# Kernel optimization log

Measured on AMD Instinct MI355X. Metric: run time of the kernel, lower is better.

## Reference

```python
import jax, jax.numpy as jnp
import numpy as np

B, C, H, W = 2, 256, 64, 64
NUM_HEADS = 8


def setup_inputs() -> dict:
    key = jax.random.key(0)
    k1, k2, k3 = jax.random.split(key, 3)
    x = jax.random.normal(k1, (B, C, H, W), dtype=jnp.float32)
    # 1x1 convs, bias=False -> plain [out_ch, in_ch] matrices
    w_qkv = jax.random.normal(k2, (3 * C, C), dtype=jnp.float32) * (1.0 / np.sqrt(C))
    w_proj = jax.random.normal(k3, (C, C), dtype=jnp.float32) * (1.0 / np.sqrt(C))
    return {"x": x, "w_qkv": w_qkv, "w_proj": w_proj}


def reference(x, w_qkv, w_proj):
    b, c, h, w = x.shape
    hd = NUM_HEADS
    d = c // hd  # head dim
    n = h * w    # number of tokens

    # 1x1 conv == channel matmul: [3C, C] x [B, C, H, W] -> [B, 3C, H, W]
    qkv = jnp.einsum('oc,bchw->bohw', w_qkv, x)
    q, k, v = jnp.split(qkv, 3, axis=1)

    def reshape(t):
        return t.reshape(b, hd, d, n)  # [B, h, d, N]

    q, k, v = map(reshape, (q, k, v))

    # scores[b,h,i,j] = sum_d q[b,h,d,i] * k[b,h,d,j] / sqrt(d)
    scores = jnp.einsum('bhdi,bhdj->bhij', q, k) / jnp.sqrt(jnp.asarray(d, x.dtype))
    attn = jax.nn.softmax(scores, axis=-1)

    # out[b,h,d,i] = sum_j attn[b,h,i,j] * v[b,h,d,j]
    out = jnp.einsum('bhij,bhdj->bhdi', attn, v)
    out = out.reshape(b, c, h, w)

    return jnp.einsum('oc,bchw->bohw', w_proj, out) + x
```

## Files before the change

### kernel.cpp

```cpp
#include <hip/hip_runtime.h>
#include <hip/hip_bf16.h>

#define NB  2
#define CC  256
#define NHD 8
#define HD  32
#define NT  4096

typedef __bf16 bf16x8 __attribute__((ext_vector_type(8)));
typedef bf16x8 bf16x8_ma __attribute__((may_alias));
typedef __bf16 bf16x4 __attribute__((ext_vector_type(4)));
typedef bf16x4 bf16x4_ma __attribute__((may_alias));
typedef float  f32x4  __attribute__((ext_vector_type(4)));
typedef float  f32x16 __attribute__((ext_vector_type(16)));
typedef unsigned int u32x4 __attribute__((ext_vector_type(4)));

static __device__ __forceinline__ f32x4 zero4() {
    f32x4 z = {0.f, 0.f, 0.f, 0.f}; return z;
}
static __device__ __forceinline__ f32x16 zero16() {
    f32x16 z = {0.f,0.f,0.f,0.f,0.f,0.f,0.f,0.f,
                0.f,0.f,0.f,0.f,0.f,0.f,0.f,0.f};
    return z;
}

#define QSCALE 0.25505392421795654f

#define CVT_PK(dst, lo, hi_) \
    asm("v_cvt_pk_bf16_f32 %0, %1, %2" : "=v"(dst) : "v"(lo), "v"(hi_))
#define PLSWAP(x, y) \
    asm("v_permlane32_swap_b32 %0, %1" : "+v"(x), "+v"(y))


__global__ __launch_bounds__(256) void convw_k(const float* __restrict__ s1,
                                               __bf16* __restrict__ d1, int n1,
                                               const float* __restrict__ s2,
                                               __bf16* __restrict__ d2, int n2) {
    const int i = blockIdx.x * 256 + threadIdx.x;
    if (i < n1) d1[i] = (__bf16)s1[i];
    else if (i - n1 < n2) d2[i - n1] = (__bf16)s2[i - n1];
}

__global__ __launch_bounds__(256) void transpose_k(const float* __restrict__ x,
                                                   __bf16* __restrict__ xt) {
    __shared__ __bf16 T[64][65];
    const int tid = threadIdx.x;
    const int n0 = blockIdx.x * 64, c0 = blockIdx.y * 64, b = blockIdx.z;

#pragma unroll
    for (int rep = 0; rep < 16; ++rep) {
        const int e = rep * 256 + tid;
        const int cl = e >> 6, nl = e & 63;
        T[nl][cl] = (__bf16)x[((size_t)(b * CC + c0 + cl)) * NT + n0 + nl];
    }
    __syncthreads();
#pragma unroll
    for (int rep = 0; rep < 16; ++rep) {
        const int e = rep * 256 + tid;
        const int nl = e >> 6, cl = e & 63;
        xt[((size_t)(b * NT + n0 + nl)) * CC + c0 + cl] = T[nl][cl];
    }
}

__global__ __launch_bounds__(256) void qkv_k(const __bf16* __restrict__ wqkv,
                                             const __bf16* __restrict__ xt,
                                             __bf16* __restrict__ qt,
                                             __bf16* __restrict__ kt,
                                             __bf16* __restrict__ vv) {
    const int lane = threadIdx.x & 63, wv = threadIdx.x >> 6;
    const int g = lane >> 4, c16 = lane & 15;
    const int b    = blockIdx.z;
    const int o0   = blockIdx.y * 64 + wv * 16;
    const int tok0 = blockIdx.x * 64;

    const __bf16* arow = wqkv + (size_t)(o0 + c16) * CC + g * 8;
    const __bf16* brow = xt + ((size_t)(b * NT + tok0 + c16)) * CC + g * 8;

    f32x4 acc[4];
#pragma unroll
    for (int i = 0; i < 4; ++i) acc[i] = zero4();

#pragma unroll
    for (int k0 = 0; k0 < CC; k0 += 32) {
        bf16x8 a = *(const bf16x8_ma*)(arow + k0);
#pragma unroll
        for (int js = 0; js < 4; ++js) {
            bf16x8 bb = *(const bf16x8_ma*)(brow + (size_t)js * 16 * CC + k0);
            acc[js] = __builtin_amdgcn_mfma_f32_16x16x32_bf16(a, bb, acc[js], 0, 0, 0);
        }
    }

    const int reg = o0 >> 8;
    const int oo0 = (o0 & 255) + g * 4;
    const int h   = oo0 >> 5;
    const int dd0 = oo0 & 31;
    const size_t bh = (size_t)(b * NHD + h);

#pragma unroll
    for (int js = 0; js < 4; ++js) {
        const int tok = tok0 + js * 16 + c16;
        if (reg == 0) {
            bf16x4 pk;
#pragma unroll
            for (int r = 0; r < 4; ++r) pk[r] = (__bf16)(acc[js][r] * QSCALE);
            *(bf16x4_ma*)(qt + (bh * NT + tok) * HD + dd0) = pk;
        } else if (reg == 1) {
            bf16x4 pk;
#pragma unroll
            for (int r = 0; r < 4; ++r) pk[r] = (__bf16)acc[js][r];
            *(bf16x4_ma*)(kt + (bh * NT + tok) * HD + dd0) = pk;
        } else {
#pragma unroll
            for (int r = 0; r < 4; ++r)
                vv[(bh * HD + dd0 + r) * NT + tok] = (__bf16)acc[js][r];
        }
    }
}

__global__ __launch_bounds__(256, 2) void attn_k(const __bf16* __restrict__ qt,
                                                 const __bf16* __restrict__ kt,
                                                 const __bf16* __restrict__ vv,
                                                 __bf16* __restrict__ ao) {
    __shared__ __align__(16) __bf16 KF[2][2][2][512];
    __shared__ __align__(16) __bf16 VF[2][2][2][512];

    const int tid  = threadIdx.x;
    const int lane = tid & 63, wv = tid >> 6;
    const int c32 = lane & 31, hi = lane >> 5;
    const int bh = blockIdx.y;
    const int b = bh >> 3, h = bh & 7;
    const int i0q = blockIdx.x * 128 + wv * 32;

    const __bf16* qbase = qt + ((size_t)bh * NT + i0q) * HD;
    const __bf16* kbase = kt + (size_t)bh * NT * HD;
    const __bf16* vbase = vv + (size_t)bh * HD * NT;

    const int stg_js = wv & 1, stg_sl = wv >> 1;

    bf16x8 aq0 = *(const bf16x8_ma*)(qbase + (size_t)c32 * HD + hi * 8);
    bf16x8 aq1 = *(const bf16x8_ma*)(qbase + (size_t)c32 * HD + 16 + hi * 8);

    f32x16 oacc = zero16();
    float rsa[4] = {0.f, 0.f, 0.f, 0.f};

#define STAGE(bf, jb) do {                                                              \
    const __bf16* gk = kbase + (size_t)((jb) + stg_js * 32 + c32) * HD                  \
                             + stg_sl * 16 + hi * 8;                                    \
    __builtin_amdgcn_global_load_lds(                                                   \
        (const __attribute__((address_space(1))) void*)gk,                              \
        (__attribute__((address_space(3))) void*)&KF[bf][stg_js][stg_sl][0],            \
        16, 0, 0);                                                                      \
    const __bf16* gv = vbase + (size_t)c32 * NT + (jb) + stg_js * 32                    \
                             + stg_sl * 16 + hi * 8;                                    \
    __builtin_amdgcn_global_load_lds(                                                   \
        (const __attribute__((address_space(1))) void*)gv,                              \
        (__attribute__((address_space(3))) void*)&VF[bf][stg_js][stg_sl][0],            \
        16, 0, 0);                                                                      \
} while (0)

#define SUBTILE(bf, js) do {                                                            \
    bf16x8 fk0 = *(const bf16x8_ma*)&KF[bf][js][0][lane * 8];                           \
    bf16x8 fk1 = *(const bf16x8_ma*)&KF[bf][js][1][lane * 8];                           \
    bf16x8 fv0 = *(const bf16x8_ma*)&VF[bf][js][0][lane * 8];                           \
    bf16x8 fv1 = *(const bf16x8_ma*)&VF[bf][js][1][lane * 8];                           \
    f32x16 s = __builtin_amdgcn_mfma_f32_32x32x16_bf16(fk0, aq0, zero16(), 0, 0, 0);    \
    s = __builtin_amdgcn_mfma_f32_32x32x16_bf16(fk1, aq1, s, 0, 0, 0);                  \
    float p[16];                                                                        \
    _Pragma("unroll")                                                                   \
    for (int r = 0; r < 16; ++r) {                                                      \
        p[r] = __builtin_amdgcn_exp2f(s[r]);                                            \
        rsa[r & 3] += p[r];                                                             \
    }                                                                                   \
    unsigned pk[8];                                                                     \
    _Pragma("unroll")                                                                   \
    for (int i = 0; i < 8; ++i) CVT_PK(pk[i], p[2 * i], p[2 * i + 1]);                  \
    PLSWAP(pk[0], pk[2]);                                                               \
    PLSWAP(pk[1], pk[3]);                                                               \
    PLSWAP(pk[4], pk[6]);                                                               \
    PLSWAP(pk[5], pk[7]);                                                               \
    u32x4 a0 = {pk[0], pk[1], pk[2], pk[3]};                                            \
    u32x4 a1 = {pk[4], pk[5], pk[6], pk[7]};                                            \
    const bf16x8 ap0 = __builtin_bit_cast(bf16x8, a0);                                  \
    const bf16x8 ap1 = __builtin_bit_cast(bf16x8, a1);                                  \
    oacc = __builtin_amdgcn_mfma_f32_32x32x16_bf16(ap0, fv0, oacc, 0, 0, 0);            \
    oacc = __builtin_amdgcn_mfma_f32_32x32x16_bf16(ap1, fv1, oacc, 0, 0, 0);            \
} while (0)

    const int NTILES = NT / 64;

    STAGE(0, 0);
    asm volatile("s_waitcnt vmcnt(0)" ::: "memory");
    __syncthreads();

    int buf = 0;
#pragma unroll 1
    for (int t = 0; t < NTILES; ++t) {
        if (t + 1 < NTILES) STAGE(buf ^ 1, (t + 1) * 64);
        SUBTILE(buf, 0);
        SUBTILE(buf, 1);
        asm volatile("s_waitcnt vmcnt(0)" ::: "memory");
        __syncthreads();
        buf ^= 1;
    }

#undef STAGE
#undef SUBTILE

    float rs = (rsa[0] + rsa[1]) + (rsa[2] + rsa[3]);
    rs += __shfl_xor(rs, 32, 64);

#pragma unroll
    for (int g4 = 0; g4 < 4; ++g4) {
#pragma unroll
        for (int r = 0; r < 4; ++r) {
            const int q = 8 * g4 + 4 * hi + r;
            const float lt = __shfl(rs, q, 64);
            ao[((size_t)(b * NT) + i0q + q) * CC + h * HD + c32] =
                (__bf16)(oacc[4 * g4 + r] / lt);
        }
    }
}

__global__ __launch_bounds__(256) void proj_k(const __bf16* __restrict__ wp,
                                              const __bf16* __restrict__ ao,
                                              const float* __restrict__ x,
                                              float* __restrict__ out) {
    const int lane = threadIdx.x & 63, wv = threadIdx.x >> 6;
    const int g = lane >> 4, c16 = lane & 15;
    const int b    = blockIdx.z;
    const int o0   = blockIdx.y * 64 + wv * 16;
    const int tok0 = blockIdx.x * 64;

    const __bf16* arow = wp + (size_t)(o0 + c16) * CC + g * 8;
    const __bf16* brow = ao + ((size_t)(b * NT + tok0 + c16)) * CC + g * 8;

    f32x4 acc[4];
#pragma unroll
    for (int i = 0; i < 4; ++i) acc[i] = zero4();

#pragma unroll
    for (int k0 = 0; k0 < CC; k0 += 32) {
        bf16x8 a = *(const bf16x8_ma*)(arow + k0);
#pragma unroll
        for (int js = 0; js < 4; ++js) {
            bf16x8 bb = *(const bf16x8_ma*)(brow + (size_t)js * 16 * CC + k0);
            acc[js] = __builtin_amdgcn_mfma_f32_16x16x32_bf16(a, bb, acc[js], 0, 0, 0);
        }
    }

#pragma unroll
    for (int js = 0; js < 4; ++js) {
        const int tok = tok0 + js * 16 + c16;
#pragma unroll
        for (int r = 0; r < 4; ++r) {
            const int o = o0 + g * 4 + r;
            const size_t idx = ((size_t)(b * CC + o)) * NT + tok;
            out[idx] = acc[js][r] + x[idx];
        }
    }
}

extern "C" void kernel_launch(void* const* d_in, const int* in_sizes, int n_in,
                              void* d_out, int out_size, void* d_ws, size_t ws_size,
                              hipStream_t stream) {
    const int SX  = NB * CC * NT;
    const int SW3 = 3 * CC * CC;
    const int SW1 = CC * CC;
    const size_t E = (size_t)SX;

    const float* x  = nullptr;
    const float* wq = nullptr;
    const float* wp = nullptr;
    for (int i = 0; i < n_in; ++i) {
        const int sz = in_sizes[i];
        if (sz == SX || sz == 2 * SX || sz == 4 * SX)           x  = (const float*)d_in[i];
        else if (sz == SW3 || sz == 2 * SW3 || sz == 4 * SW3)   wq = (const float*)d_in[i];
        else if (sz == SW1 || sz == 2 * SW1 || sz == 4 * SW1)   wp = (const float*)d_in[i];
    }
    if (!x || !wq || !wp) {
        x  = (const float*)d_in[0];
        wq = (const float*)d_in[1];
        wp = (const float*)d_in[2];
    }

    __bf16* ws  = (__bf16*)d_ws;
    __bf16* wqb = ws;
    __bf16* wpb = wqb + SW3;
    __bf16* xt  = wpb + SW1;
    __bf16* qt  = xt + E;
    __bf16* kt  = qt + E;
    __bf16* vv  = kt + E;
    __bf16* ao  = xt;

    float* out = (float*)d_out;

    convw_k<<<dim3((SW3 + SW1 + 255) / 256), 256, 0, stream>>>(wq, wqb, SW3, wp, wpb, SW1);
    transpose_k<<<dim3(NT / 64, CC / 64, NB), 256, 0, stream>>>(x, xt);
    qkv_k<<<dim3(NT / 64, (3 * CC) / 64, NB), 256, 0, stream>>>(wqb, xt, qt, kt, vv);
    attn_k<<<dim3(NT / 128, NB * NHD), 256, 0, stream>>>(qt, kt, vv, ao);
    proj_k<<<dim3(NT / 64, CC / 64, NB), 256, 0, stream>>>(wpb, ao, x, out);
}
```

Before: 166.5 us.

## Deepen attention K/V pipeline to four buffers and stage GEMM operands in LDS

The attention kernel moves from double-buffered to quad-buffered K/V LDS staging, keeping three tiles in flight. It waits with partial vmcnt counts and raw s_barrier, and raises wave priority around the MFMA work. The qkv and proj GEMMs now load the shared token tile once per block into LDS via global_load_lds, so the four waves no longer each re-read it from global memory, and they preload all weight fragments into registers. This targets load latency stalls in exchange for more LDS per block, which may lower occupancy in attention, and tighter hand-tuned wait counts.

```diff
diff --git a/kernel.cpp b/kernel.cpp
--- a/kernel.cpp
+++ b/kernel.cpp
@@ -67,26 +67,40 @@
                                              __bf16* __restrict__ qt,
                                              __bf16* __restrict__ kt,
                                              __bf16* __restrict__ vv) {
+    __shared__ __align__(16) __bf16 BF[4][8][512];
+
     const int lane = threadIdx.x & 63, wv = threadIdx.x >> 6;
     const int g = lane >> 4, c16 = lane & 15;
     const int b    = blockIdx.z;
     const int o0   = blockIdx.y * 64 + wv * 16;
     const int tok0 = blockIdx.x * 64;
 
+    const __bf16* bsrc = xt + ((size_t)(b * NT + tok0 + wv * 16 + c16)) * CC + g * 8;
+#pragma unroll
+    for (int kc = 0; kc < 8; ++kc) {
+        __builtin_amdgcn_global_load_lds(
+            (const __attribute__((address_space(1))) void*)(bsrc + kc * 32),
+            (__attribute__((address_space(3))) void*)&BF[wv][kc][0],
+            16, 0, 0);
+    }
+
     const __bf16* arow = wqkv + (size_t)(o0 + c16) * CC + g * 8;
-    const __bf16* brow = xt + ((size_t)(b * NT + tok0 + c16)) * CC + g * 8;
+    bf16x8 a[8];
+#pragma unroll
+    for (int kc = 0; kc < 8; ++kc) a[kc] = *(const bf16x8_ma*)(arow + kc * 32);
+
+    __syncthreads();
 
     f32x4 acc[4];
 #pragma unroll
     for (int i = 0; i < 4; ++i) acc[i] = zero4();
 
 #pragma unroll
-    for (int k0 = 0; k0 < CC; k0 += 32) {
-        bf16x8 a = *(const bf16x8_ma*)(arow + k0);
+    for (int kc = 0; kc < 8; ++kc) {
 #pragma unroll
         for (int js = 0; js < 4; ++js) {
-            bf16x8 bb = *(const bf16x8_ma*)(brow + (size_t)js * 16 * CC + k0);
-            acc[js] = __builtin_amdgcn_mfma_f32_16x16x32_bf16(a, bb, acc[js], 0, 0, 0);
+            bf16x8 bb = *(const bf16x8_ma*)&BF[js][kc][lane * 8];
+            acc[js] = __builtin_amdgcn_mfma_f32_16x16x32_bf16(a[kc], bb, acc[js], 0, 0, 0);
         }
     }
 
@@ -121,8 +135,8 @@
                                                  const __bf16* __restrict__ kt,
                                                  const __bf16* __restrict__ vv,
                                                  __bf16* __restrict__ ao) {
-    __shared__ __align__(16) __bf16 KF[2][2][2][512];
-    __shared__ __align__(16) __bf16 VF[2][2][2][512];
+    __shared__ __align__(16) __bf16 KF[4][2][2][512];
+    __shared__ __align__(16) __bf16 VF[4][2][2][512];
 
     const int tid  = threadIdx.x;
     const int lane = tid & 63, wv = tid >> 6;
@@ -186,25 +200,47 @@
     oacc = __builtin_amdgcn_mfma_f32_32x32x16_bf16(ap1, fv1, oacc, 0, 0, 0);            \
 } while (0)
 
+#define TILE_WAIT(VMC) do {                                                             \
+    __builtin_amdgcn_sched_barrier(0);                                                  \
+    asm volatile("s_waitcnt vmcnt(" #VMC ")" ::: "memory");                             \
+    __builtin_amdgcn_s_barrier();                                                       \
+    asm volatile("" ::: "memory");                                                      \
+    __builtin_amdgcn_sched_barrier(0);                                                  \
+} while (0)
+
     const int NTILES = NT / 64;
 
     STAGE(0, 0);
-    asm volatile("s_waitcnt vmcnt(0)" ::: "memory");
-    __syncthreads();
-
-    int buf = 0;
+    STAGE(1, 64);
+    STAGE(2, 128);
+    __builtin_amdgcn_sched_barrier(0);
+
+    int t = 0;
 #pragma unroll 1
-    for (int t = 0; t < NTILES; ++t) {
-        if (t + 1 < NTILES) STAGE(buf ^ 1, (t + 1) * 64);
-        SUBTILE(buf, 0);
-        SUBTILE(buf, 1);
-        asm volatile("s_waitcnt vmcnt(0)" ::: "memory");
-        __syncthreads();
-        buf ^= 1;
-    }
+    for (; t < NTILES - 3; ++t) {
+        TILE_WAIT(4);
+        STAGE((t + 3) & 3, (t + 3) * 64);
+        __builtin_amdgcn_s_setprio(1);
+        SUBTILE(t & 3, 0);
+        SUBTILE(t & 3, 1);
+        __builtin_amdgcn_s_setprio(0);
+    }
+    TILE_WAIT(4);
+    __builtin_amdgcn_s_setprio(1);
+    SUBTILE(61 & 3, 0); SUBTILE(61 & 3, 1);
+    __builtin_amdgcn_s_setprio(0);
+    TILE_WAIT(2);
+    __builtin_amdgcn_s_setprio(1);
+    SUBTILE(62 & 3, 0); SUBTILE(62 & 3, 1);
+    __builtin_amdgcn_s_setprio(0);
+    TILE_WAIT(0);
+    __builtin_amdgcn_s_setprio(1);
+    SUBTILE(63 & 3, 0); SUBTILE(63 & 3, 1);
+    __builtin_amdgcn_s_setprio(0);
 
 #undef STAGE
 #undef SUBTILE
+#undef TILE_WAIT
 
     float rs = (rsa[0] + rsa[1]) + (rsa[2] + rsa[3]);
     rs += __shfl_xor(rs, 32, 64);
@@ -225,26 +261,40 @@
                                               const __bf16* __restrict__ ao,
                                               const float* __restrict__ x,
                                               float* __restrict__ out) {
+    __shared__ __align__(16) __bf16 BF[4][8][512];
+
     const int lane = threadIdx.x & 63, wv = threadIdx.x >> 6;
     const int g = lane >> 4, c16 = lane & 15;
     const int b    = blockIdx.z;
     const int o0   = blockIdx.y * 64 + wv * 16;
     const int tok0 = blockIdx.x * 64;
 
+    const __bf16* bsrc = ao + ((size_t)(b * NT + tok0 + wv * 16 + c16)) * CC + g * 8;
+#pragma unroll
+    for (int kc = 0; kc < 8; ++kc) {
+        __builtin_amdgcn_global_load_lds(
+            (const __attribute__((address_space(1))) void*)(bsrc + kc * 32),
+            (__attribute__((address_space(3))) void*)&BF[wv][kc][0],
+            16, 0, 0);
+    }
+
     const __bf16* arow = wp + (size_t)(o0 + c16) * CC + g * 8;
-    const __bf16* brow = ao + ((size_t)(b * NT + tok0 + c16)) * CC + g * 8;
+    bf16x8 a[8];
+#pragma unroll
+    for (int kc = 0; kc < 8; ++kc) a[kc] = *(const bf16x8_ma*)(arow + kc * 32);
+
+    __syncthreads();
 
     f32x4 acc[4];
 #pragma unroll
     for (int i = 0; i < 4; ++i) acc[i] = zero4();
 
 #pragma unroll
-    for (int k0 = 0; k0 < CC; k0 += 32) {
-        bf16x8 a = *(const bf16x8_ma*)(arow + k0);
+    for (int kc = 0; kc < 8; ++kc) {
 #pragma unroll
         for (int js = 0; js < 4; ++js) {
-            bf16x8 bb = *(const bf16x8_ma*)(brow + (size_t)js * 16 * CC + k0);
-            acc[js] = __builtin_amdgcn_mfma_f32_16x16x32_bf16(a, bb, acc[js], 0, 0, 0);
+            bf16x8 bb = *(const bf16x8_ma*)&BF[js][kc][lane * 8];
+            acc[js] = __builtin_amdgcn_mfma_f32_16x16x32_bf16(a[kc], bb, acc[js], 0, 0, 0);
         }
     }
 
```

Measured after the change: 151.7 us. 1.1x faster.
